# Kernel tuning notes

Measured on AMD Instinct MI355X. Metric: run time of the kernel, lower is better.

Reference implementation:

```python
import jax, jax.numpy as jnp
import numpy as np

K = 64
P = 13               # int(1 + 0.2 * K), module default
KP = K + P - 1       # truncation degree of the polynomial
N_S = 2048
N_C = 10000
NEG = -1e9           # finite stand-in for -inf (log of zero coefficient); keeps vjp NaN-free


def setup_inputs() -> dict:
    key = jax.random.key(0)
    x = jax.random.normal(key, (N_S, N_C), dtype=jnp.float32)
    return {"x": x}


def _log_esp(x, kp):
    """Log elementary symmetric polynomials of exp(x) along the class axis.

    x: (n_s, n_c). Returns L of shape (kp+1, n_s) with
    L[j, s] = log sigma_j(exp(x[s, :])), exactly the truncated log-domain
    polynomial product prod_i (1 + exp(x_i) t) that the torch module computes
    via divide-and-conquer.
    """
    n_s, n_c = x.shape
    # carry: log-coefficients of the partial product, degrees 0..kp
    init = jnp.full((kp + 1, n_s), NEG, dtype=x.dtype).at[0].set(0.0)
    pad = jnp.full((1, n_s), NEG, dtype=x.dtype)

    def step(L, xi):
        # multiply partial polynomial by (1 + exp(xi) t), truncated at degree kp
        shifted = jnp.concatenate([pad, L[:-1] + xi[None, :]], axis=0)
        return jnp.logaddexp(L, shifted), None

    L, _ = jax.lax.scan(step, init, x.T)  # scan over n_c classes
    return L


def reference(x):
    coeff = _log_esp(x, KP)          # (kp+1, n_s)
    return coeff[K - 1:K + 1]        # (2, n_s): log sigma_{k-1}, log sigma_k
```

## Files before the change

kernel.cpp:

```cpp
#include <hip/hip_runtime.h>


#define NS 2048
#define NC 10000
#define KSEL 64

__global__ __launch_bounds__(256, 4)
void logesp_kernel(const float* __restrict__ x, float* __restrict__ out) {
  __shared__ float W2[64 * 28];
  __shared__ float W3[32 * 37];
  __shared__ float W4[16 * 53];
  __shared__ float W5[8 * 77];
  __shared__ float W6[4 * 109];
  __shared__ float W7[2 * 70];
  __shared__ float scLog[64];
  __shared__ float red[8];

  const int t  = threadIdx.x;
  const int wv = t >> 6;
  const int s  = blockIdx.x;

  const float4* xv = (const float4*)(x + (size_t)s * NC);
  float4 buf[10];
#pragma unroll
  for (int it = 0; it < 9; ++it) buf[it] = xv[t + it * 256];
  buf[9] = make_float4(-1e30f, -1e30f, -1e30f, -1e30f);
  if (t < 196) buf[9] = xv[2304 + t];

  float c0 = 1.f, c1 = 0.f, c2 = 0.f, c3 = 0.f, c4 = 0.f, c5 = 0.f, c6 = 0.f;
  float sw = 0.f;
#pragma unroll
  for (int it = 0; it < 10; ++it) {
    const float4 v = buf[it];
#pragma unroll
    for (int q = 0; q < 4; ++q) {
      const float xval = q == 0 ? v.x : q == 1 ? v.y : q == 2 ? v.z : v.w;
      const float w = __expf(xval);
      sw += w;
      c6 = fmaf(w, c5, c6);
      c5 = fmaf(w, c4, c5);
      c4 = fmaf(w, c3, c4);
      c3 = fmaf(w, c2, c3);
      c2 = fmaf(w, c1, c2);
      c1 = fmaf(w, c0, c1);
    }
  }

#pragma unroll
  for (int m = 1; m < 64; m <<= 1) sw += __shfl_xor(sw, m);
  if ((t & 63) == 0) red[wv] = sw;
  __syncthreads();
  const float wsum = red[0] + red[1] + red[2] + red[3];
  const float tau = __logf(wsum * ((float)(NC - KSEL) / ((float)KSEL * (float)NC)));

  {
    const float f1 = __expf(-tau);
    const float f2 = f1 * f1, f3 = f2 * f1, f4v = f2 * f2, f5 = f4v * f1, f6 = f4v * f2;
    c1 *= f1; c2 *= f2; c3 *= f3; c4 *= f4v; c5 *= f5; c6 *= f6;
  }
  {
    const float mx = fmaxf(fmaxf(fmaxf(c0, c1), fmaxf(c2, c3)), fmaxf(fmaxf(c4, c5), c6));
    const float invm = 1.f / mx;
    c0 *= invm; c1 *= invm; c2 *= invm; c3 *= invm; c4 *= invm; c5 *= invm; c6 *= invm;
    float Sr = __logf(mx);
#pragma unroll
    for (int m = 1; m < 64; m <<= 1) Sr += __shfl_xor(Sr, m);
    if ((t & 63) == 0) red[4 + wv] = Sr;
  }

  const float q0 = __shfl_xor(c0, 1), q1 = __shfl_xor(c1, 1), q2 = __shfl_xor(c2, 1),
              q3 = __shfl_xor(c3, 1), q4 = __shfl_xor(c4, 1), q5 = __shfl_xor(c5, 1),
              q6 = __shfl_xor(c6, 1);
  const float e0 = c0 * q0;
  const float e1 = fmaf(c1, q0, c0 * q1);
  const float e2 = fmaf(c2, q0, fmaf(c1, q1, c0 * q2));
  const float e3 = fmaf(c3, q0, fmaf(c2, q1, fmaf(c1, q2, c0 * q3)));
  const float e4 = fmaf(c4, q0, fmaf(c3, q1, fmaf(c2, q2, fmaf(c1, q3, c0 * q4))));
  const float e5 = fmaf(c5, q0, fmaf(c4, q1, fmaf(c3, q2, fmaf(c2, q3, fmaf(c1, q4, c0 * q5)))));
  const float e6 = fmaf(c6, q0, fmaf(c5, q1, fmaf(c4, q2, fmaf(c3, q3, fmaf(c2, q4, fmaf(c1, q5, c0 * q6))))));
  const float e7 = fmaf(c6, q1, fmaf(c5, q2, fmaf(c4, q3, fmaf(c3, q4, fmaf(c2, q5, c1 * q6)))));

  const float f0 = __shfl_xor(e0, 2), f1 = __shfl_xor(e1, 2), f2 = __shfl_xor(e2, 2),
              f3 = __shfl_xor(e3, 2), f4 = __shfl_xor(e4, 2), f5 = __shfl_xor(e5, 2),
              f6 = __shfl_xor(e6, 2), f7 = __shfl_xor(e7, 2);
  const float g0 = e0 * f0;
  const float g1 = fmaf(e1, f0, e0 * f1);
  const float g2 = fmaf(e2, f0, fmaf(e1, f1, e0 * f2));
  const float g3 = fmaf(e3, f0, fmaf(e2, f1, fmaf(e1, f2, e0 * f3)));
  const float g4 = fmaf(e4, f0, fmaf(e3, f1, fmaf(e2, f2, fmaf(e1, f3, e0 * f4))));
  const float g5 = fmaf(e5, f0, fmaf(e4, f1, fmaf(e3, f2, fmaf(e2, f3, fmaf(e1, f4, e0 * f5)))));
  const float g6 = fmaf(e6, f0, fmaf(e5, f1, fmaf(e4, f2, fmaf(e3, f3, fmaf(e2, f4, fmaf(e1, f5, e0 * f6))))));
  const float g7 = fmaf(e7, f0, fmaf(e6, f1, fmaf(e5, f2, fmaf(e4, f3, fmaf(e3, f4, fmaf(e2, f5, fmaf(e1, f6, e0 * f7)))))));
  const float g8 = fmaf(e7, f1, fmaf(e6, f2, fmaf(e5, f3, fmaf(e4, f4, fmaf(e3, f5, fmaf(e2, f6, e1 * f7))))));
  const float g9 = fmaf(e7, f2, fmaf(e6, f3, fmaf(e5, f4, fmaf(e4, f5, fmaf(e3, f6, e2 * f7)))));
  const float g10 = fmaf(e7, f3, fmaf(e6, f4, fmaf(e5, f5, fmaf(e4, f6, e3 * f7))));
  const float g11 = fmaf(e7, f4, fmaf(e6, f5, fmaf(e5, f6, e4 * f7)));

  if ((t & 3) == 0) {
    float* row = W2 + (t >> 2) * 28;
    *(float4*)(row)      = make_float4(0.f, 0.f, 0.f, 0.f);
    *(float4*)(row + 4)  = make_float4(0.f, 0.f, 0.f, 0.f);
    *(float4*)(row + 8)  = make_float4(0.f, 0.f, 0.f, g0);
    *(float4*)(row + 12) = make_float4(g1, g2, g3, g4);
    *(float4*)(row + 16) = make_float4(g5, g6, g7, g8);
    *(float4*)(row + 20) = make_float4(g9, g10, g11, 0.f);
    *(float4*)(row + 24) = make_float4(0.f, 0.f, 0.f, 0.f);
  }

  {
    const int m = t >> 3, r = t & 7;
    const float* A = W2 + (2 * m) * 28;
    const float* B = W2 + (2 * m + 1) * 28;
    float o0 = 0.f, o1 = 0.f, o2 = 0.f;
#pragma unroll
    for (int i = 0; i <= 11; ++i) {
      const float ai = A[11 + i];
      o0 = fmaf(ai, B[11 + r - i], o0);
      o1 = fmaf(ai, B[19 + r - i], o1);
      o2 = fmaf(ai, B[27 - i], o2);
    }
    float mx = fmaxf(fmaxf(o0, o1), o2);
    mx = fmaxf(mx, __shfl_xor(mx, 1));
    mx = fmaxf(mx, __shfl_xor(mx, 2));
    mx = fmaxf(mx, __shfl_xor(mx, 4));
    const float inv = 1.f / mx;
    float* O = W3 + m * 37;
    O[16 + r] = o0 * inv;
    O[24 + r] = o1 * inv;
    if (r == 0) { O[32] = o2 * inv; scLog[m] = __logf(mx); }
    O[r] = 0.f; O[8 + r] = 0.f;
    if (r < 4) O[33 + r] = 0.f;
  }

  {
    const int m = t >> 4, r = t & 15;
    const float* A = W3 + (2 * m) * 37;
    const float* B = W3 + (2 * m + 1) * 37;
    float o0 = 0.f, o1 = 0.f;
#pragma unroll
    for (int i = 0; i <= 16; ++i) {
      const float ai = A[16 + i];
      o0 = fmaf(ai, B[16 + r - i], o0);
      o1 = fmaf(ai, B[32 + r - i], o1);
    }
    if (r >= 5) o1 = 0.f;
    float mx = fmaxf(o0, o1);
    mx = fmaxf(mx, __shfl_xor(mx, 1));
    mx = fmaxf(mx, __shfl_xor(mx, 2));
    mx = fmaxf(mx, __shfl_xor(mx, 4));
    mx = fmaxf(mx, __shfl_xor(mx, 8));
    const float inv = 1.f / mx;
    float* O = W4 + m * 53;
    O[20 + r] = o0 * inv;
    if (r < 5) O[36 + r] = o1 * inv;
    if (r == 0) scLog[32 + m] = __logf(mx);
    O[r] = 0.f;
    if (r < 4) O[16 + r] = 0.f;
    if (r < 12) O[41 + r] = 0.f;
  }

  {
    const int m = t >> 5, p = t & 31;
    const float* A = W4 + (2 * m) * 53;
    const float* B = W4 + (2 * m + 1) * 53;
    float o0 = 0.f, o1 = 0.f;
#pragma unroll
    for (int i = 0; i <= 20; ++i) {
      const float ai = A[20 + i];
      o0 = fmaf(ai, B[20 + p - i], o0);
      o1 = fmaf(ai, B[52 - i], o1);
    }
    float mx = fmaxf(o0, o1);
    mx = fmaxf(mx, __shfl_xor(mx, 1));
    mx = fmaxf(mx, __shfl_xor(mx, 2));
    mx = fmaxf(mx, __shfl_xor(mx, 4));
    mx = fmaxf(mx, __shfl_xor(mx, 8));
    mx = fmaxf(mx, __shfl_xor(mx, 16));
    const float inv = 1.f / mx;
    float* O = W5 + m * 77;
    O[32 + p] = o0 * inv;
    if (p == 0) { O[64] = o1 * inv; scLog[48 + m] = __logf(mx); }
    O[p] = 0.f;
    if (p < 12) O[65 + p] = 0.f;
  }

  {
    const int p = t & 63;
    const float* A = W5 + (2 * wv) * 77;
    const float* B = W5 + (2 * wv + 1) * 77;
    float o0 = 0.f;
#pragma unroll
    for (int i = 0; i <= 32; ++i) {
      const float ai = A[32 + i];
      o0 = fmaf(ai, B[32 + p - i], o0);
    }
    if (p >= 45) o0 = 0.f;
    float mx = o0;
#pragma unroll
    for (int msk = 1; msk < 64; msk <<= 1) mx = fmaxf(mx, __shfl_xor(mx, msk));
    const float inv = 1.f / mx;
    float* O = W6 + wv * 109;
    if (p < 45) O[44 + p] = o0 * inv;
    if (p == 0) scLog[56 + wv] = __logf(mx);
    if (p < 44) O[p] = 0.f;
    if (p < 20) O[89 + p] = 0.f;
  }
  __syncthreads();

  if (t < 128) {
    const int p = t & 63;
    const float* A = W6 + (2 * wv) * 109;
    const float* B = W6 + (2 * wv + 1) * 109;
    float o0 = 0.f, o1 = 0.f;
#pragma unroll
    for (int i = 0; i <= 44; ++i) {
      const float ai = A[44 + i];
      o0 = fmaf(ai, B[44 + p - i], o0);
      o1 = fmaf(ai, B[108 - i], o1);
    }
    float mx = fmaxf(o0, o1);
#pragma unroll
    for (int msk = 1; msk < 64; msk <<= 1) mx = fmaxf(mx, __shfl_xor(mx, msk));
    const float inv = 1.f / mx;
    float* O = W7 + wv * 70;
    O[p] = o0 * inv;
    if (p == 0) { O[64] = o1 * inv; scLog[60 + wv] = __logf(mx); }
  }
  __syncthreads();

  if (t < 64) {
    const float* A = W7;
    const float* B = W7 + 70;
    const float a = A[t];
    float v63 = a * B[63 - t];
    float v64 = a * B[64 - t];
    float ee = (t < 62) ? scLog[t] : 0.f;
#pragma unroll
    for (int msk = 1; msk < 64; msk <<= 1) {
      v63 += __shfl_xor(v63, msk);
      v64 += __shfl_xor(v64, msk);
      ee  += __shfl_xor(ee, msk);
    }
    if (t == 0) {
      v64 = fmaf(A[64], B[0], v64);
      const float Ssum = red[4] + red[5] + red[6] + red[7] + ee;
      out[s]      = __logf(v63) + Ssum + 63.f * tau;
      out[NS + s] = __logf(v64) + Ssum + 64.f * tau;
    }
  }
}

extern "C" void kernel_launch(void* const* d_in, const int* in_sizes, int n_in,
                              void* d_out, int out_size, void* d_ws, size_t ws_size,
                              hipStream_t stream) {
  const float* x = (const float*)d_in[0];
  float* out = (float*)d_out;
  (void)in_sizes; (void)n_in; (void)d_ws; (void)ws_size; (void)out_size;
  logesp_kernel<<<NS, 256, 0, stream>>>(x, out);
}
```

Measured before the change: 29.52 us.

## Register-tile the tree-convolution stages with float4 LDS loads and drop a barrier

Each polynomial-product stage of the log-ESP tree now computes four output coefficients per thread. It reads operands as float4 from a single padded shared-memory buffer, which cuts scalar LDS loads and most of the idle lanes. The whole buffer is zeroed once at kernel start instead of writing zero padding in every stage. The second-to-last stage now runs entirely in wave 0, feeding the last stage directly, so one __syncthreads is removed. In exchange, correctness now depends on the up-front zeroing being ordered before the first stage writes, and on the new padded offsets being right.

```diff
diff --git a/kernel.cpp b/kernel.cpp
--- a/kernel.cpp
+++ b/kernel.cpp
@@ -5,20 +5,43 @@
 #define NC 10000
 #define KSEL 64
 
+#define OW2 0
+#define OW3 2048
+#define OW4 3456
+#define OW5 4416
+#define OW6 5088
+#define OW7 5552
+#define LDSF 5688
+
+__device__ __forceinline__ float4 ld4(const float* p) { return *(const float4*)p; }
+__device__ __forceinline__ void st4(float* p, float a, float b, float c, float d) {
+  *(float4*)p = make_float4(a, b, c, d);
+}
+
+#define CONV4(a4, bl, bh)                                                               \
+  a0 = fmaf(a4.x, bh.x, a0); a1 = fmaf(a4.x, bh.y, a1); a2 = fmaf(a4.x, bh.z, a2); a3 = fmaf(a4.x, bh.w, a3); \
+  a0 = fmaf(a4.y, bl.w, a0); a1 = fmaf(a4.y, bh.x, a1); a2 = fmaf(a4.y, bh.y, a2); a3 = fmaf(a4.y, bh.z, a3); \
+  a0 = fmaf(a4.z, bl.z, a0); a1 = fmaf(a4.z, bl.w, a1); a2 = fmaf(a4.z, bh.x, a2); a3 = fmaf(a4.z, bh.y, a3); \
+  a0 = fmaf(a4.w, bl.y, a0); a1 = fmaf(a4.w, bl.z, a1); a2 = fmaf(a4.w, bl.w, a2); a3 = fmaf(a4.w, bh.x, a3)
+
 __global__ __launch_bounds__(256, 4)
 void logesp_kernel(const float* __restrict__ x, float* __restrict__ out) {
-  __shared__ float W2[64 * 28];
-  __shared__ float W3[32 * 37];
-  __shared__ float W4[16 * 53];
-  __shared__ float W5[8 * 77];
-  __shared__ float W6[4 * 109];
-  __shared__ float W7[2 * 70];
+  __shared__ float LW[LDSF];
   __shared__ float scLog[64];
   __shared__ float red[8];
 
   const int t  = threadIdx.x;
   const int wv = t >> 6;
   const int s  = blockIdx.x;
+
+  {
+    float4* z4 = (float4*)LW;
+#pragma unroll
+    for (int u = 0; u < 6; ++u) {
+      const int idx = t + u * 256;
+      if (idx < LDSF / 4) z4[idx] = make_float4(0.f, 0.f, 0.f, 0.f);
+    }
+  }
 
   const float4* xv = (const float4*)(x + (size_t)s * NC);
   float4 buf[10];
@@ -97,140 +120,145 @@
   const float g11 = fmaf(e7, f4, fmaf(e6, f5, fmaf(e5, f6, e4 * f7)));
 
   if ((t & 3) == 0) {
-    float* row = W2 + (t >> 2) * 28;
-    *(float4*)(row)      = make_float4(0.f, 0.f, 0.f, 0.f);
-    *(float4*)(row + 4)  = make_float4(0.f, 0.f, 0.f, 0.f);
-    *(float4*)(row + 8)  = make_float4(0.f, 0.f, 0.f, g0);
-    *(float4*)(row + 12) = make_float4(g1, g2, g3, g4);
-    *(float4*)(row + 16) = make_float4(g5, g6, g7, g8);
-    *(float4*)(row + 20) = make_float4(g9, g10, g11, 0.f);
-    *(float4*)(row + 24) = make_float4(0.f, 0.f, 0.f, 0.f);
+    float* row = LW + OW2 + (t >> 2) * 32;
+    st4(row + 12, g0, g1, g2, g3);
+    st4(row + 16, g4, g5, g6, g7);
+    st4(row + 20, g8, g9, g10, g11);
   }
 
   {
     const int m = t >> 3, r = t & 7;
-    const float* A = W2 + (2 * m) * 28;
-    const float* B = W2 + (2 * m + 1) * 28;
-    float o0 = 0.f, o1 = 0.f, o2 = 0.f;
-#pragma unroll
-    for (int i = 0; i <= 11; ++i) {
-      const float ai = A[11 + i];
-      o0 = fmaf(ai, B[11 + r - i], o0);
-      o1 = fmaf(ai, B[19 + r - i], o1);
-      o2 = fmaf(ai, B[27 - i], o2);
-    }
-    float mx = fmaxf(fmaxf(o0, o1), o2);
-    mx = fmaxf(mx, __shfl_xor(mx, 1));
-    mx = fmaxf(mx, __shfl_xor(mx, 2));
-    mx = fmaxf(mx, __shfl_xor(mx, 4));
-    const float inv = 1.f / mx;
-    float* O = W3 + m * 37;
-    O[16 + r] = o0 * inv;
-    O[24 + r] = o1 * inv;
-    if (r == 0) { O[32] = o2 * inv; scLog[m] = __logf(mx); }
-    O[r] = 0.f; O[8 + r] = 0.f;
-    if (r < 4) O[33 + r] = 0.f;
+    const float* A = LW + OW2 + (2 * m) * 32 + 12;
+    const float* B = LW + OW2 + (2 * m + 1) * 32 + 12;
+    float a0 = 0.f, a1 = 0.f, a2 = 0.f, a3 = 0.f;
+    const int j0 = 4 * r;
+    if (r < 5) {
+#pragma unroll
+      for (int i0 = 0; i0 <= 8; i0 += 4) {
+        const float4 a4 = ld4(A + i0);
+        const float4 bl = ld4(B + j0 - i0 - 4);
+        const float4 bh = ld4(B + j0 - i0);
+        CONV4(a4, bl, bh);
+      }
+      if (r == 4) { a1 = 0.f; a2 = 0.f; a3 = 0.f; }
+    }
+    float mx = fmaxf(fmaxf(a0, a1), fmaxf(a2, a3));
+    mx = fmaxf(mx, __shfl_xor(mx, 1));
+    mx = fmaxf(mx, __shfl_xor(mx, 2));
+    mx = fmaxf(mx, __shfl_xor(mx, 4));
+    const float inv = 1.f / mx;
+    if (r < 5) st4(LW + OW3 + m * 44 + 20 + j0, a0 * inv, a1 * inv, a2 * inv, a3 * inv);
+    if (r == 0) scLog[m] = __logf(mx);
   }
 
   {
     const int m = t >> 4, r = t & 15;
-    const float* A = W3 + (2 * m) * 37;
-    const float* B = W3 + (2 * m + 1) * 37;
-    float o0 = 0.f, o1 = 0.f;
-#pragma unroll
-    for (int i = 0; i <= 16; ++i) {
-      const float ai = A[16 + i];
-      o0 = fmaf(ai, B[16 + r - i], o0);
-      o1 = fmaf(ai, B[32 + r - i], o1);
-    }
-    if (r >= 5) o1 = 0.f;
-    float mx = fmaxf(o0, o1);
+    const float* A = LW + OW3 + (2 * m) * 44 + 20;
+    const float* B = LW + OW3 + (2 * m + 1) * 44 + 20;
+    float a0 = 0.f, a1 = 0.f, a2 = 0.f, a3 = 0.f;
+    const int j0 = 4 * r;
+    if (r < 6) {
+#pragma unroll
+      for (int i0 = 0; i0 <= 16; i0 += 4) {
+        const float4 a4 = ld4(A + i0);
+        const float4 bl = ld4(B + j0 - i0 - 4);
+        const float4 bh = ld4(B + j0 - i0);
+        CONV4(a4, bl, bh);
+      }
+      if (r == 5) { a1 = 0.f; a2 = 0.f; a3 = 0.f; }
+    }
+    float mx = fmaxf(fmaxf(a0, a1), fmaxf(a2, a3));
     mx = fmaxf(mx, __shfl_xor(mx, 1));
     mx = fmaxf(mx, __shfl_xor(mx, 2));
     mx = fmaxf(mx, __shfl_xor(mx, 4));
     mx = fmaxf(mx, __shfl_xor(mx, 8));
     const float inv = 1.f / mx;
-    float* O = W4 + m * 53;
-    O[20 + r] = o0 * inv;
-    if (r < 5) O[36 + r] = o1 * inv;
+    if (r < 6) st4(LW + OW4 + m * 60 + 24 + j0, a0 * inv, a1 * inv, a2 * inv, a3 * inv);
     if (r == 0) scLog[32 + m] = __logf(mx);
-    O[r] = 0.f;
-    if (r < 4) O[16 + r] = 0.f;
-    if (r < 12) O[41 + r] = 0.f;
-  }
-
-  {
-    const int m = t >> 5, p = t & 31;
-    const float* A = W4 + (2 * m) * 53;
-    const float* B = W4 + (2 * m + 1) * 53;
-    float o0 = 0.f, o1 = 0.f;
-#pragma unroll
-    for (int i = 0; i <= 20; ++i) {
-      const float ai = A[20 + i];
-      o0 = fmaf(ai, B[20 + p - i], o0);
-      o1 = fmaf(ai, B[52 - i], o1);
-    }
-    float mx = fmaxf(o0, o1);
+  }
+
+  {
+    const int m = t >> 5, r = t & 31;
+    const float* A = LW + OW4 + (2 * m) * 60 + 24;
+    const float* B = LW + OW4 + (2 * m + 1) * 60 + 24;
+    float a0 = 0.f, a1 = 0.f, a2 = 0.f, a3 = 0.f;
+    const int j0 = 4 * r;
+    if (r < 9) {
+#pragma unroll
+      for (int i0 = 0; i0 <= 20; i0 += 4) {
+        const float4 a4 = ld4(A + i0);
+        const float4 bl = ld4(B + j0 - i0 - 4);
+        const float4 bh = ld4(B + j0 - i0);
+        CONV4(a4, bl, bh);
+      }
+      if (r == 8) { a1 = 0.f; a2 = 0.f; a3 = 0.f; }
+    }
+    float mx = fmaxf(fmaxf(a0, a1), fmaxf(a2, a3));
     mx = fmaxf(mx, __shfl_xor(mx, 1));
     mx = fmaxf(mx, __shfl_xor(mx, 2));
     mx = fmaxf(mx, __shfl_xor(mx, 4));
     mx = fmaxf(mx, __shfl_xor(mx, 8));
     mx = fmaxf(mx, __shfl_xor(mx, 16));
     const float inv = 1.f / mx;
-    float* O = W5 + m * 77;
-    O[32 + p] = o0 * inv;
-    if (p == 0) { O[64] = o1 * inv; scLog[48 + m] = __logf(mx); }
-    O[p] = 0.f;
-    if (p < 12) O[65 + p] = 0.f;
-  }
-
-  {
-    const int p = t & 63;
-    const float* A = W5 + (2 * wv) * 77;
-    const float* B = W5 + (2 * wv + 1) * 77;
-    float o0 = 0.f;
-#pragma unroll
-    for (int i = 0; i <= 32; ++i) {
-      const float ai = A[32 + i];
-      o0 = fmaf(ai, B[32 + p - i], o0);
-    }
-    if (p >= 45) o0 = 0.f;
-    float mx = o0;
+    if (r < 9) st4(LW + OW5 + m * 84 + 36 + j0, a0 * inv, a1 * inv, a2 * inv, a3 * inv);
+    if (r == 0) scLog[48 + m] = __logf(mx);
+  }
+
+  {
+    const int r = t & 63;
+    const float* A = LW + OW5 + (2 * wv) * 84 + 36;
+    const float* B = LW + OW5 + (2 * wv + 1) * 84 + 36;
+    float a0 = 0.f, a1 = 0.f, a2 = 0.f, a3 = 0.f;
+    const int j0 = 4 * r;
+    if (r < 12) {
+#pragma unroll
+      for (int i0 = 0; i0 <= 32; i0 += 4) {
+        const float4 a4 = ld4(A + i0);
+        const float4 bl = ld4(B + j0 - i0 - 4);
+        const float4 bh = ld4(B + j0 - i0);
+        CONV4(a4, bl, bh);
+      }
+      if (r == 11) { a1 = 0.f; a2 = 0.f; a3 = 0.f; }
+    }
+    float mx = fmaxf(fmaxf(a0, a1), fmaxf(a2, a3));
 #pragma unroll
     for (int msk = 1; msk < 64; msk <<= 1) mx = fmaxf(mx, __shfl_xor(mx, msk));
     const float inv = 1.f / mx;
-    float* O = W6 + wv * 109;
-    if (p < 45) O[44 + p] = o0 * inv;
-    if (p == 0) scLog[56 + wv] = __logf(mx);
-    if (p < 44) O[p] = 0.f;
-    if (p < 20) O[89 + p] = 0.f;
+    if (r < 12) st4(LW + OW6 + wv * 116 + 48 + j0, a0 * inv, a1 * inv, a2 * inv, a3 * inv);
+    if (r == 0) scLog[56 + wv] = __logf(mx);
   }
   __syncthreads();
 
-  if (t < 128) {
-    const int p = t & 63;
-    const float* A = W6 + (2 * wv) * 109;
-    const float* B = W6 + (2 * wv + 1) * 109;
-    float o0 = 0.f, o1 = 0.f;
-#pragma unroll
-    for (int i = 0; i <= 44; ++i) {
-      const float ai = A[44 + i];
-      o0 = fmaf(ai, B[44 + p - i], o0);
-      o1 = fmaf(ai, B[108 - i], o1);
-    }
-    float mx = fmaxf(o0, o1);
-#pragma unroll
-    for (int msk = 1; msk < 64; msk <<= 1) mx = fmaxf(mx, __shfl_xor(mx, msk));
-    const float inv = 1.f / mx;
-    float* O = W7 + wv * 70;
-    O[p] = o0 * inv;
-    if (p == 0) { O[64] = o1 * inv; scLog[60 + wv] = __logf(mx); }
-  }
-  __syncthreads();
-
   if (t < 64) {
-    const float* A = W7;
-    const float* B = W7 + 70;
+    const int m = (t >> 5) & 1, r = t & 31;
+    const float* A = LW + OW6 + (2 * m) * 116 + 48;
+    const float* B = LW + OW6 + (2 * m + 1) * 116 + 48;
+    float a0 = 0.f, a1 = 0.f, a2 = 0.f, a3 = 0.f;
+    const int j0 = 4 * r;
+    if (r < 17) {
+#pragma unroll
+      for (int i0 = 0; i0 <= 44; i0 += 4) {
+        const float4 a4 = ld4(A + i0);
+        const float4 bl = ld4(B + j0 - i0 - 4);
+        const float4 bh = ld4(B + j0 - i0);
+        CONV4(a4, bl, bh);
+      }
+      if (r == 16) { a1 = 0.f; a2 = 0.f; a3 = 0.f; }
+    }
+    float mx = fmaxf(fmaxf(a0, a1), fmaxf(a2, a3));
+    mx = fmaxf(mx, __shfl_xor(mx, 1));
+    mx = fmaxf(mx, __shfl_xor(mx, 2));
+    mx = fmaxf(mx, __shfl_xor(mx, 4));
+    mx = fmaxf(mx, __shfl_xor(mx, 8));
+    mx = fmaxf(mx, __shfl_xor(mx, 16));
+    const float inv = 1.f / mx;
+    if (r < 17) st4(LW + OW7 + m * 68 + j0, a0 * inv, a1 * inv, a2 * inv, a3 * inv);
+    if (r == 0) scLog[60 + m] = __logf(mx);
+  }
+
+  if (t < 64) {
+    const float* A = LW + OW7;
+    const float* B = LW + OW7 + 68;
     const float a = A[t];
     float v63 = a * B[63 - t];
     float v64 = a * B[64 - t];
```

Result: slower. 31.63 us (+7.2%).
